# Optimization experiments

Hardware: AMD Instinct MI355X
Metric: run time of the kernel (lower is better)

The kernel has to match this reference:

```python
import jax, jax.numpy as jnp
import numpy as np

B, L, H, D, N, R, K = 1, 2048, 2048, 4096, 16, 128, 4


def setup_inputs() -> dict:
    key = jax.random.key(0)
    ks = jax.random.split(key, 10)
    s = 0.02
    x = jax.random.normal(ks[0], (B, L, H), dtype=jnp.float32)
    W_in = jax.random.normal(ks[1], (H, 2 * D), dtype=jnp.float32) * s
    conv_w = jax.random.normal(ks[2], (K, D), dtype=jnp.float32) * s  # depthwise causal conv
    conv_b = jnp.zeros((D,), dtype=jnp.float32)
    W_x = jax.random.normal(ks[3], (D, R + 2 * N), dtype=jnp.float32) * s
    W_dt = jax.random.normal(ks[4], (R, D), dtype=jnp.float32) * (R ** -0.5)
    # dt bias initialized so softplus(b_dt) ~ dt in [1e-3, 1e-1]
    dt = jnp.exp(jax.random.uniform(ks[5], (D,)) * (np.log(0.1) - np.log(1e-3)) + np.log(1e-3))
    b_dt = dt + jnp.log(-jnp.expm1(-dt))
    A_log = jnp.broadcast_to(jnp.log(jnp.arange(1, N + 1, dtype=jnp.float32)), (D, N))
    D_param = jnp.ones((D,), dtype=jnp.float32)
    W_out = jax.random.normal(ks[6], (D, H), dtype=jnp.float32) * s
    return {"x": x, "W_in": W_in, "conv_w": conv_w, "conv_b": conv_b,
            "W_x": W_x, "W_dt": W_dt, "b_dt": b_dt, "A_log": A_log,
            "D_param": D_param, "W_out": W_out}


def _mamba_fwd(x, W_in, conv_w, conv_b, W_x, W_dt, b_dt, A_log, D_param, W_out):
    silu = jax.nn.silu
    # in_proj then chunk into hidden / gate: [B,L,D] each
    proj = x @ W_in
    hs, gate = jnp.split(proj, 2, axis=-1)
    # causal depthwise conv along sequence (pad K-1 on the left)
    hs_pad = jnp.pad(hs, ((0, 0), (K - 1, 0), (0, 0)))
    conv = sum(hs_pad[:, k:k + L, :] * conv_w[k] for k in range(K)) + conv_b
    hs = silu(conv)  # [B,L,D]
    # ssm parameters
    ssm_p = hs @ W_x  # [B,L,R+2N]
    dt_in, Bm, Cm = jnp.split(ssm_p, [R, R + N], axis=-1)
    dt = jax.nn.softplus(dt_in @ W_dt + b_dt)  # [B,L,D]
    A = -jnp.exp(A_log)  # [D,N]
    dA = jnp.exp(dt[..., None] * A)                       # [B,L,D,N]
    dBu = dt[..., None] * Bm[:, :, None, :] * hs[..., None]  # [B,L,D,N]

    def step(s, inp):
        dA_t, dBu_t, C_t = inp
        s = dA_t * s + dBu_t                 # [B,D,N]
        y = jnp.einsum('bdn,bn->bd', s, C_t)
        return s, y

    s0 = jnp.zeros((B, D, N), dtype=x.dtype)
    xs = (jnp.moveaxis(dA, 1, 0), jnp.moveaxis(dBu, 1, 0), jnp.moveaxis(Cm, 1, 0))
    _, ys = jax.lax.scan(step, s0, xs)       # [L,B,D]
    y = jnp.moveaxis(ys, 0, 1)               # [B,L,D]
    y = y + hs * D_param
    y = y * silu(gate)
    return y @ W_out                          # [B,L,H]


def reference(x, W_in, conv_w, conv_b, W_x, W_dt, b_dt, A_log, D_param, W_out):
    return _mamba_fwd(x, W_in, conv_w, conv_b, W_x, W_dt, b_dt, A_log, D_param, W_out)
```

## Files before the change

### kernel.cpp

```cpp
#include <hip/hip_runtime.h>
#include <hip/hip_bf16.h>

typedef short short8 __attribute__((ext_vector_type(8)));
typedef float floatx4 __attribute__((ext_vector_type(4)));
using bf16 = __hip_bfloat16;

static constexpr int L = 2048, H = 2048, D = 4096, NS = 16, R = 128, KC = 4;
static constexpr int CCH = 64, TCH = L / CCH;
static constexpr int KSP = 16, KCHUNK = 4096 / KSP;
static constexpr int ZOUT = 4, KOUT = 4096 / ZOUT;

__device__ __forceinline__ void g2lds16(const void* g, void* l) {
  __builtin_amdgcn_global_load_lds((const __attribute__((address_space(1))) unsigned int*)g,
                                   (__attribute__((address_space(3))) unsigned int*)l,
                                   16, 0, 0);
}

__global__ void cast_f2b(const float* __restrict__ in, bf16* __restrict__ out, int n) {
  int i = blockIdx.x * 256 + threadIdx.x;
  if (i < n) out[i] = __float2bfloat16(in[i]);
}

__global__ void transpose_cast(const float* __restrict__ in, bf16* __restrict__ out,
                               int Rr, int Cc) {
  __shared__ float tile[32][33];
  int c0 = blockIdx.x * 32, r0 = blockIdx.y * 32;
  int tx = threadIdx.x, ty = threadIdx.y;
#pragma unroll
  for (int i = 0; i < 32; i += 8)
    tile[ty + i][tx] = in[(size_t)(r0 + ty + i) * Cc + (c0 + tx)];
  __syncthreads();
#pragma unroll
  for (int i = 0; i < 32; i += 8)
    out[(size_t)(c0 + ty + i) * Rr + (r0 + tx)] = __float2bfloat16(tile[tx][ty + i]);
}

template <int MODE>
__global__ __launch_bounds__(512, 2) void gemm256(
    const bf16* __restrict__ A, int lda,
    const bf16* __restrict__ Bt, int ldb,
    bf16* __restrict__ Cb, bf16* __restrict__ Cb2, int ldc, int K) {
  __shared__ short As[4 * 8192];
  __shared__ short Bs[4 * 8192];

  const int gx = gridDim.x, gy = gridDim.y;
  const int orig = blockIdx.y * gx + blockIdx.x;
  const int xcd = orig & 7;
  const int rr = orig >> 3;
  const int rn = gx >> 2, rm = gy >> 1;
  const int tn = (xcd & 3) * rn + (rr % rn);
  const int tm = (xcd >> 2) * rm + (rr / rn);
  const int n0 = tn * 256, m0 = tm * 256;
  const int kbeg = (MODE == 3) ? blockIdx.z * K : 0;
  const int NT = K >> 6;

  const int tid = threadIdx.x;
  const int lane = tid & 63;
  const int w = tid >> 6;
  const int wm2 = w >> 2, wn4 = w & 3;
  const int lr = lane & 15, kq = lane >> 4;
  const int swzr = ((lane >> 3) & 1) << 1;
  const int ardo = (wm2 * 128 + lr) * 32 + (kq ^ swzr) * 8;
  const int brdo = (wn4 * 64 + lr) * 32 + (kq ^ swzr) * 8;
  const int srow = w * 16 + (lane >> 2);
  const int swzs = ((lane >> 5) & 1) << 1;
  const int scol = ((lane & 3) ^ swzs) * 8;

  floatx4 acc[8][4];
#pragma unroll
  for (int i = 0; i < 8; i++)
#pragma unroll
    for (int j = 0; j < 4; j++)
#pragma unroll
      for (int r = 0; r < 4; r++) acc[i][j][r] = 0.f;

  auto stageA = [&](short* pan, int kc) {
    const bf16* g = A + (size_t)(m0 + srow) * lda + (kbeg + kc + scol);
    g2lds16(g, pan + w * 512);
    g2lds16(g + (size_t)128 * lda, pan + 4096 + w * 512);
  };
  auto stageB = [&](short* pan, int kc) {
    const bf16* g = Bt + (size_t)(n0 + srow) * ldb + (kbeg + kc + scol);
    g2lds16(g, pan + w * 512);
    g2lds16(g + (size_t)128 * ldb, pan + 4096 + w * 512);
  };

#define LDA4(pan, base)                                               \
  _Pragma("unroll") for (int ii = 0; ii < 4; ii++)                    \
      af[ii] = *(const short8*)((pan) + ardo + ((base) + ii) * 512);
#define LDB4(pan)                                                     \
  _Pragma("unroll") for (int jj = 0; jj < 4; jj++)                    \
      bfr[jj] = *(const short8*)((pan) + brdo + jj * 512);
#define MFMA4(base)                                                   \
  _Pragma("unroll") for (int ii = 0; ii < 4; ii++)                    \
      _Pragma("unroll") for (int jj = 0; jj < 4; jj++)                \
          acc[(base) + ii][jj] = __builtin_amdgcn_mfma_f32_16x16x32_bf16( \
              af[ii], bfr[jj], acc[(base) + ii][jj], 0, 0, 0);
#define LGK0() asm volatile("s_waitcnt lgkmcnt(0)" ::: "memory");
#define VMW(n) asm volatile("s_waitcnt vmcnt(" #n ")" ::: "memory");
#define BAR() __builtin_amdgcn_s_barrier();

  stageA(As + 0 * 8192, 0);
  stageB(Bs + 0 * 8192, 0);
  stageA(As + 1 * 8192, 32);
  stageB(Bs + 1 * 8192, 32);
  stageA(As + 2 * 8192, 64);
  stageB(Bs + 2 * 8192, 64);
  VMW(8);
  BAR();

#define GTILE(t, par)                                                      \
  {                                                                        \
    short* Ak0 = As + (par) * 16384;                                       \
    short* Bk0 = Bs + (par) * 16384;                                       \
    short* Ak1 = Ak0 + 8192;                                               \
    short* Bk1 = Bk0 + 8192;                                               \
    short* An1 = As + (1 - (par)) * 16384 + 8192;                          \
    short* Bn1 = Bs + (1 - (par)) * 16384 + 8192;                          \
    short8 af[4], bfr[4];                                                  \
                                                \
    LDB4(Bk0); LDA4(Ak0, 0);                                               \
    if ((t) + 1 < NT) stageA(An1, ((t) + 1) * 64 + 32);                    \
    __builtin_amdgcn_s_setprio(1); MFMA4(0); __builtin_amdgcn_s_setprio(0);\
    BAR();                                                                 \
                                   \
    LDA4(Ak0, 4);                                                          \
    if ((t) + 1 < NT) stageB(Bn1, ((t) + 1) * 64 + 32);                    \
    __builtin_amdgcn_s_setprio(1); MFMA4(4); __builtin_amdgcn_s_setprio(0);\
    LGK0();                                                                \
    if ((t) < NT - 1) { VMW(8); } else { VMW(0); }      \
    BAR();                                                                 \
                                                \
    LDB4(Bk1); LDA4(Ak1, 0);                                               \
    if ((t) + 2 < NT) stageA(Ak0, ((t) + 2) * 64);                         \
    __builtin_amdgcn_s_setprio(1); MFMA4(0); __builtin_amdgcn_s_setprio(0);\
    BAR();                                                                 \
                                   \
    LDA4(Ak1, 4);                                                          \
    if ((t) + 2 < NT) stageB(Bk0, ((t) + 2) * 64);                         \
    __builtin_amdgcn_s_setprio(1); MFMA4(4); __builtin_amdgcn_s_setprio(0);\
    LGK0();                                                                \
                                                      \
    if ((t) < NT - 2) { VMW(8); }                                          \
    else if ((t) == NT - 2) { VMW(4); }                                    \
    else { VMW(0); }                                                       \
    BAR();                                                                 \
  }

  for (int t = 0; t < NT; t += 2) {
    GTILE(t, 0);
    GTILE(t + 1, 1);
  }
#undef GTILE
#undef BAR
#undef VMW
#undef LGK0
#undef MFMA4
#undef LDB4
#undef LDA4

  bf16* base = Cb;
  int coff = 0, ld = ldc;
  if (MODE == 2) {
    if (n0 >= D) { base = Cb2; coff = D; }
    ld = D;
  }
  if (MODE == 3) base = Cb + (size_t)blockIdx.z * L * ldc;
  const int rb = kq * 4;
#pragma unroll
  for (int i = 0; i < 8; i++)
#pragma unroll
    for (int j = 0; j < 4; j++) {
      int col = n0 + wn4 * 64 + j * 16 + lr - coff;
      int row = m0 + wm2 * 128 + i * 16 + rb;
#pragma unroll
      for (int r = 0; r < 4; r++)
        base[(size_t)(row + r) * ld + col] = __float2bfloat16(acc[i][j][r]);
    }
}

template <int MODE>
__global__ __launch_bounds__(256) void gemm_async(
    const bf16* __restrict__ A, int lda,
    const bf16* __restrict__ Bt, int ldb,
    bf16* __restrict__ Cb, bf16* __restrict__ Cb2, int ldc, int K) {
  __shared__ short As[2 * 128 * 32];
  __shared__ short Bs[2 * 128 * 32];
  const int m0 = blockIdx.y * 128, n0 = blockIdx.x * 128;
  const int kbeg = (MODE == 3) ? blockIdx.z * K : 0;
  const int tid = threadIdx.x;
  const int lane = tid & 63;
  const int wave = tid >> 6;
  const int wm = (wave >> 1) * 64, wn = (wave & 1) * 64;
  const int lr = lane & 15, kq = lane >> 4;
  const int sr = lane >> 2, sc = (lane & 3) * 8;

  const bf16* Ab = A + (size_t)(m0 + wave * 16 + sr) * lda + sc;
  const bf16* Bb = Bt + (size_t)(n0 + wave * 16 + sr) * ldb + sc;
  short* Asw = &As[wave * 16 * 32];
  short* Bsw = &Bs[wave * 16 * 32];

  floatx4 acc[4][4];
#pragma unroll
  for (int i = 0; i < 4; i++)
#pragma unroll
    for (int j = 0; j < 4; j++)
#pragma unroll
      for (int r = 0; r < 4; r++) acc[i][j][r] = 0.f;

  for (int k0 = kbeg; k0 < kbeg + K; k0 += 64) {
    __syncthreads();
#pragma unroll
    for (int h = 0; h < 2; h++) {
      int kk = k0 + h * 32;
#pragma unroll
      for (int j = 0; j < 2; j++) {
        g2lds16(Ab + (size_t)j * 64 * lda + kk, Asw + h * 4096 + j * 64 * 32);
        g2lds16(Bb + (size_t)j * 64 * ldb + kk, Bsw + h * 4096 + j * 64 * 32);
      }
    }
    __syncthreads();
#pragma unroll
    for (int h = 0; h < 2; h++) {
      short8 af[4], bfr[4];
#pragma unroll
      for (int i = 0; i < 4; i++)
        af[i] = *(const short8*)(&As[h * 4096 + (wm + i * 16 + lr) * 32 + kq * 8]);
#pragma unroll
      for (int j = 0; j < 4; j++)
        bfr[j] = *(const short8*)(&Bs[h * 4096 + (wn + j * 16 + lr) * 32 + kq * 8]);
#pragma unroll
      for (int i = 0; i < 4; i++)
#pragma unroll
        for (int j = 0; j < 4; j++)
          acc[i][j] = __builtin_amdgcn_mfma_f32_16x16x32_bf16(af[i], bfr[j], acc[i][j], 0, 0, 0);
    }
  }

  bf16* base = Cb;
  int coff = 0, ld = ldc;
  if (MODE == 2) {
    if (n0 >= D) { base = Cb2; coff = D; }
    ld = D;
  }
  if (MODE == 3) base = Cb + (size_t)blockIdx.z * L * ldc;
  const int rb = kq * 4;
#pragma unroll
  for (int i = 0; i < 4; i++)
#pragma unroll
    for (int j = 0; j < 4; j++) {
      int col = n0 + wn + j * 16 + lr - coff;
      int row = m0 + wm + i * 16 + rb;
#pragma unroll
      for (int r = 0; r < 4; r++)
        base[(size_t)(row + r) * ld + col] = __float2bfloat16(acc[i][j][r]);
    }
}

__global__ void out_reduce(const unsigned short* __restrict__ P, float* __restrict__ out) {
  int i = blockIdx.x * 256 + threadIdx.x;
  const size_t LH = (size_t)L * H;
  float acc[8];
#pragma unroll
  for (int e = 0; e < 8; e++) acc[e] = 0.f;
#pragma unroll
  for (int z = 0; z < ZOUT; z++) {
    short8 v = *(const short8*)(P + z * LH + (size_t)i * 8);
#pragma unroll
    for (int e = 0; e < 8; e++)
      acc[e] += __uint_as_float(((unsigned)(unsigned short)v[e]) << 16);
  }
#pragma unroll
  for (int q = 0; q < 2; q++) {
    floatx4 o;
#pragma unroll
    for (int r = 0; r < 4; r++) o[r] = acc[q * 4 + r];
    *(floatx4*)(out + (size_t)i * 8 + q * 4) = o;
  }
}

__global__ __launch_bounds__(256) void gemm_splitk(
    const bf16* __restrict__ A, int lda,
    const bf16* __restrict__ Bt, int ldb,
    float* __restrict__ P, int ldc, int N) {
  __shared__ short As[128 * 40];
  __shared__ short Bs[128 * 40];
  const int m0 = blockIdx.y * 128, n0 = blockIdx.x * 128;
  const int kbeg = blockIdx.z * KCHUNK;
  float* C = P + (size_t)blockIdx.z * L * ldc;
  const int tid = threadIdx.x;
  const int lane = tid & 63;
  const int wave = tid >> 6;
  const int wm = (wave >> 1) * 64, wn = (wave & 1) * 64;
  const int lr = lane & 15, kq = lane >> 4;
  const int srow = tid >> 2, scol = (tid & 3) * 8;

  floatx4 acc[4][4];
#pragma unroll
  for (int i = 0; i < 4; i++)
#pragma unroll
    for (int j = 0; j < 4; j++)
#pragma unroll
      for (int r = 0; r < 4; r++) acc[i][j][r] = 0.f;

  for (int k0 = kbeg; k0 < kbeg + KCHUNK; k0 += 32) {
    __syncthreads();
#pragma unroll
    for (int h = 0; h < 2; h++) {
      int r = srow + h * 64;
      short8 va = *(const short8*)((const short*)A + (size_t)(m0 + r) * lda + k0 + scol);
      *(short8*)(&As[r * 40 + scol]) = va;
    }
#pragma unroll
    for (int h = 0; h < 2; h++) {
      int r = srow + h * 64;
      short8 vb;
      if ((n0 + r) < N) {
        vb = *(const short8*)((const short*)Bt + (size_t)(n0 + r) * ldb + k0 + scol);
      } else {
#pragma unroll
        for (int q = 0; q < 8; q++) vb[q] = 0;
      }
      *(short8*)(&Bs[r * 40 + scol]) = vb;
    }
    __syncthreads();
    short8 af[4], bfr[4];
#pragma unroll
    for (int i = 0; i < 4; i++)
      af[i] = *(const short8*)(&As[(wm + i * 16 + lr) * 40 + kq * 8]);
#pragma unroll
    for (int j = 0; j < 4; j++)
      bfr[j] = *(const short8*)(&Bs[(wn + j * 16 + lr) * 40 + kq * 8]);
#pragma unroll
    for (int i = 0; i < 4; i++)
#pragma unroll
      for (int j = 0; j < 4; j++)
        acc[i][j] = __builtin_amdgcn_mfma_f32_16x16x32_bf16(af[i], bfr[j], acc[i][j], 0, 0, 0);
  }

  const int rb = kq * 4;
#pragma unroll
  for (int i = 0; i < 4; i++)
#pragma unroll
    for (int j = 0; j < 4; j++) {
      int col = n0 + wn + j * 16 + lr;
      if (col >= N) continue;
      int row = m0 + wm + i * 16 + rb;
#pragma unroll
      for (int r = 0; r < 4; r++)
        C[(size_t)(row + r) * ldc + col] = acc[i][j][r];
    }
}

__global__ void splitk_reduce(const float* __restrict__ P, float* __restrict__ ssmp,
                              bf16* __restrict__ dtin) {
  int idx = blockIdx.x * 256 + threadIdx.x;
  float s = 0.f;
#pragma unroll
  for (int z = 0; z < KSP; z++) s += P[(size_t)z * L * 160 + idx];
  ssmp[idx] = s;
  int t = idx / 160, c = idx - t * 160;
  if (c < R) dtin[t * R + c] = __float2bfloat16(s);
}

__global__ void conv_silu(const bf16* __restrict__ projh,
                          const float* __restrict__ conv_w, const float* __restrict__ conv_b,
                          bf16* __restrict__ hs_b) {
  int idx = blockIdx.x * 256 + threadIdx.x;
  int d = idx & (D - 1), t = idx >> 12;
  float acc = conv_b[d];
#pragma unroll
  for (int k = 0; k < KC; k++) {
    int tt = t + k - (KC - 1);
    if (tt >= 0) acc += __bfloat162float(projh[(size_t)tt * D + d]) * conv_w[k * D + d];
  }
  float s = acc / (1.f + __expf(-acc));
  hs_b[idx] = __float2bfloat16(s);
}

__device__ __forceinline__ float softplusf(float v) {
  return (v > 20.f) ? v : log1pf(__expf(v));
}

__global__ __launch_bounds__(256) void scan_phase1(
    const bf16* __restrict__ dtraw, const float* __restrict__ b_dt,
    const bf16* __restrict__ hs_b, const float* __restrict__ ssmp,
    const float* __restrict__ A_log,
    float* __restrict__ sdt_out, float* __restrict__ S_out) {
  const int d = blockIdx.x * 256 + threadIdx.x;
  const int c = blockIdx.y;
  float An[NS];
#pragma unroll
  for (int n = 0; n < NS; n++) An[n] = -__expf(A_log[d * NS + n]);
  const float bdt = b_dt[d];
  float s[NS];
#pragma unroll
  for (int n = 0; n < NS; n++) s[n] = 0.f;
  float sdt = 0.f;
  const int t0 = c * TCH;
#pragma unroll 2
  for (int t = t0; t < t0 + TCH; t++) {
    float dtv = softplusf(__bfloat162float(dtraw[(size_t)t * D + d]) + bdt);
    float hsv = __bfloat162float(hs_b[(size_t)t * D + d]);
    sdt += dtv;
    float u = dtv * hsv;
    const float* Bp = ssmp + (size_t)t * 160 + 128;
#pragma unroll
    for (int n = 0; n < NS; n++) {
      float dA = __expf(An[n] * dtv);
      s[n] = dA * s[n] + Bp[n] * u;
    }
  }
  sdt_out[(size_t)c * D + d] = sdt;
  float* Sp = S_out + ((size_t)c * D + d) * NS;
#pragma unroll
  for (int n = 0; n < NS; n += 4)
    *(floatx4*)(Sp + n) = *(floatx4*)(s + n);
}

__global__ __launch_bounds__(256) void scan_phase2(
    const float* __restrict__ sdt, const float* __restrict__ S,
    const float* __restrict__ A_log, float* __restrict__ I) {
  int g = blockIdx.x * 256 + threadIdx.x;
  int d = g >> 4;
  float An = -__expf(A_log[g]);
  float cur = 0.f;
  float sdt_n = sdt[d];
  float S_n = S[g];
  for (int c = 0; c < CCH; c++) {
    float sdt_c = sdt_n, S_c = S_n;
    if (c + 1 < CCH) {
      sdt_n = sdt[(size_t)(c + 1) * D + d];
      S_n = S[(size_t)(c + 1) * D * NS + g];
    }
    I[(size_t)c * D * NS + g] = cur;
    cur = __expf(An * sdt_c) * cur + S_c;
  }
}

__global__ __launch_bounds__(256) void scan_phase3(
    const bf16* __restrict__ dtraw, const float* __restrict__ b_dt,
    const bf16* __restrict__ hs_b, const float* __restrict__ ssmp,
    const bf16* __restrict__ gate_b, const float* __restrict__ A_log,
    const float* __restrict__ D_param, const float* __restrict__ I,
    bf16* __restrict__ y_b) {
  const int d = blockIdx.x * 256 + threadIdx.x;
  const int c = blockIdx.y;
  float An[NS];
#pragma unroll
  for (int n = 0; n < NS; n++) An[n] = -__expf(A_log[d * NS + n]);
  const float bdt = b_dt[d];
  const float Dp = D_param[d];
  float s[NS];
  const float* Ip = I + ((size_t)c * D + d) * NS;
#pragma unroll
  for (int n = 0; n < NS; n += 4)
    *(floatx4*)(s + n) = *(const floatx4*)(Ip + n);
  const int t0 = c * TCH;
#pragma unroll 2
  for (int t = t0; t < t0 + TCH; t++) {
    float dtv = softplusf(__bfloat162float(dtraw[(size_t)t * D + d]) + bdt);
    float hsv = __bfloat162float(hs_b[(size_t)t * D + d]);
    float u = dtv * hsv;
    const float* Bp = ssmp + (size_t)t * 160 + 128;
    const float* Cp = ssmp + (size_t)t * 160 + 144;
    float y = 0.f;
#pragma unroll
    for (int n = 0; n < NS; n++) {
      float dA = __expf(An[n] * dtv);
      s[n] = dA * s[n] + Bp[n] * u;
      y += s[n] * Cp[n];
    }
    float gv = __bfloat162float(gate_b[(size_t)t * D + d]);
    float yv = (y + hsv * Dp) * (gv / (1.f + __expf(-gv)));
    y_b[(size_t)t * D + d] = __float2bfloat16(yv);
  }
}

extern "C" void kernel_launch(void* const* d_in, const int* in_sizes, int n_in,
                              void* d_out, int out_size, void* d_ws, size_t ws_size,
                              hipStream_t stream) {
  const float* x      = (const float*)d_in[0];
  const float* W_in   = (const float*)d_in[1];
  const float* conv_w = (const float*)d_in[2];
  const float* conv_b = (const float*)d_in[3];
  const float* W_x    = (const float*)d_in[4];
  const float* W_dt   = (const float*)d_in[5];
  const float* b_dt   = (const float*)d_in[6];
  const float* A_log  = (const float*)d_in[7];
  const float* D_par  = (const float*)d_in[8];
  const float* W_out  = (const float*)d_in[9];
  float* outp = (float*)d_out;

  char* ws = (char*)d_ws;
  size_t off = 0;
  auto alloc = [&](size_t bytes) {
    char* p = ws + off;
    off += (bytes + 255) & ~(size_t)255;
    return (void*)p;
  };
  bf16*  gate_b  = (bf16*) alloc((size_t)L * D * 2);
  bf16*  hs_b    = (bf16*) alloc((size_t)L * D * 2);
  float* ssmp    = (float*)alloc((size_t)L * 160 * 4);
  bf16*  dtin_b  = (bf16*) alloc((size_t)L * R * 2);
  bf16*  dtbuf_b = (bf16*) alloc((size_t)L * D * 2);
  bf16*  y_b     = (bf16*) alloc((size_t)L * D * 2);
  bf16*  WoutT   = (bf16*) alloc((size_t)H * D * 2);
  float* sdt     = (float*)alloc((size_t)CCH * D * 4);
  float* Sbuf    = (float*)alloc((size_t)CCH * D * NS * 4);
  float* Ibuf    = (float*)alloc((size_t)CCH * D * NS * 4);
  size_t tbase = off;
  bf16*  x_b     = (bf16*) alloc((size_t)L * H * 2);
  bf16*  WinT    = (bf16*) alloc((size_t)2 * D * H * 2);
  bf16*  WxT     = (bf16*) alloc((size_t)160 * D * 2);
  bf16*  WdtT    = (bf16*) alloc((size_t)D * R * 2);
  bf16*  projh_b = (bf16*) alloc((size_t)L * D * 2);
  float* part    = (float*)alloc((size_t)KSP * L * 160 * 4);
  bf16*  part2   = (bf16*)(ws + tbase);

  cast_f2b<<<(L * H) / 256, 256, 0, stream>>>(x, x_b, L * H);

  dim3 tb(32, 8);
  transpose_cast<<<dim3((2 * D) / 32, H / 32), tb, 0, stream>>>(W_in, WinT, H, 2 * D);
  transpose_cast<<<dim3(H / 32, D / 32), tb, 0, stream>>>(W_out, WoutT, D, H);
  transpose_cast<<<dim3(160 / 32, D / 32), tb, 0, stream>>>(W_x, WxT, D, 160);
  transpose_cast<<<dim3(D / 32, R / 32), tb, 0, stream>>>(W_dt, WdtT, R, D);

  gemm256<2><<<dim3((2 * D) / 256, L / 256), 512, 0, stream>>>(
      x_b, H, WinT, H, projh_b, gate_b, D, H);
  conv_silu<<<(L * D) / 256, 256, 0, stream>>>(projh_b, conv_w, conv_b, hs_b);
  gemm_splitk<<<dim3(2, L / 128, KSP), 256, 0, stream>>>(
      hs_b, D, WxT, D, part, 160, 160);
  splitk_reduce<<<(L * 160) / 256, 256, 0, stream>>>(part, ssmp, dtin_b);
  gemm_async<1><<<dim3(D / 128, L / 128), 256, 0, stream>>>(
      dtin_b, R, WdtT, R, dtbuf_b, nullptr, D, R);

  scan_phase1<<<dim3(D / 256, CCH), 256, 0, stream>>>(
      dtbuf_b, b_dt, hs_b, ssmp, A_log, sdt, Sbuf);
  scan_phase2<<<(D * NS) / 256, 256, 0, stream>>>(sdt, Sbuf, A_log, Ibuf);
  scan_phase3<<<dim3(D / 256, CCH), 256, 0, stream>>>(
      dtbuf_b, b_dt, hs_b, ssmp, gate_b, A_log, D_par, Ibuf, y_b);

  gemm256<3><<<dim3(H / 256, L / 256, ZOUT), 512, 0, stream>>>(
      y_b, D, WoutT, D, part2, nullptr, H, KOUT);
  out_reduce<<<(L * H) / (256 * 8), 256, 0, stream>>>((const unsigned short*)part2, outp);
}
```

Measured before the change: 472.5 us.

## Restructure GEMM main loop into four-stage ring with one barrier pair per k-slice

Replaces the two-half-tile GTILE schedule (split A loads and four barriers per 32-wide k-slice) with a four-slot LDS ring. Each phase waits on vmcnt, loads all 8 A fragments and 4 B fragments, issues the next global-to-LDS stage into a free slot, then runs all 32 MFMAs at once. This aims to cut barrier count and interleaving overhead in the large bf16 GEMMs. The cost is more live A registers and less fine-grained overlap of LDS reads with MFMAs, and the vmcnt accounting at the loop tail has to stay correct.

```diff
diff --git a/kernel.cpp b/kernel.cpp
--- a/kernel.cpp
+++ b/kernel.cpp
@@ -85,79 +85,55 @@
     g2lds16(g + (size_t)128 * ldb, pan + 4096 + w * 512);
   };
 
-#define LDA4(pan, base)                                               \
-  _Pragma("unroll") for (int ii = 0; ii < 4; ii++)                    \
-      af[ii] = *(const short8*)((pan) + ardo + ((base) + ii) * 512);
+#define LDA8(pan)                                                     \
+  _Pragma("unroll") for (int ii = 0; ii < 8; ii++)                    \
+      af[ii] = *(const short8*)((pan) + ardo + ii * 512);
 #define LDB4(pan)                                                     \
   _Pragma("unroll") for (int jj = 0; jj < 4; jj++)                    \
       bfr[jj] = *(const short8*)((pan) + brdo + jj * 512);
-#define MFMA4(base)                                                   \
-  _Pragma("unroll") for (int ii = 0; ii < 4; ii++)                    \
+#define MFMA32()                                                      \
+  _Pragma("unroll") for (int ii = 0; ii < 8; ii++)                    \
       _Pragma("unroll") for (int jj = 0; jj < 4; jj++)                \
-          acc[(base) + ii][jj] = __builtin_amdgcn_mfma_f32_16x16x32_bf16( \
-              af[ii], bfr[jj], acc[(base) + ii][jj], 0, 0, 0);
+          acc[ii][jj] = __builtin_amdgcn_mfma_f32_16x16x32_bf16(      \
+              af[ii], bfr[jj], acc[ii][jj], 0, 0, 0);
 #define LGK0() asm volatile("s_waitcnt lgkmcnt(0)" ::: "memory");
 #define VMW(n) asm volatile("s_waitcnt vmcnt(" #n ")" ::: "memory");
 #define BAR() __builtin_amdgcn_s_barrier();
 
-  stageA(As + 0 * 8192, 0);
-  stageB(Bs + 0 * 8192, 0);
-  stageA(As + 1 * 8192, 32);
-  stageB(Bs + 1 * 8192, 32);
-  stageA(As + 2 * 8192, 64);
-  stageB(Bs + 2 * 8192, 64);
-  VMW(8);
-  BAR();
-
-#define GTILE(t, par)                                                      \
+  stageA(As + 0 * 8192, 0);   stageB(Bs + 0 * 8192, 0);
+  stageA(As + 1 * 8192, 32);  stageB(Bs + 1 * 8192, 32);
+  stageA(As + 2 * 8192, 64);  stageB(Bs + 2 * 8192, 64);
+
+#define GPH(sR, sS, kcS, vmn, scond)                                       \
   {                                                                        \
-    short* Ak0 = As + (par) * 16384;                                       \
-    short* Bk0 = Bs + (par) * 16384;                                       \
-    short* Ak1 = Ak0 + 8192;                                               \
-    short* Bk1 = Bk0 + 8192;                                               \
-    short* An1 = As + (1 - (par)) * 16384 + 8192;                          \
-    short* Bn1 = Bs + (1 - (par)) * 16384 + 8192;                          \
-    short8 af[4], bfr[4];                                                  \
-                                                \
-    LDB4(Bk0); LDA4(Ak0, 0);                                               \
-    if ((t) + 1 < NT) stageA(An1, ((t) + 1) * 64 + 32);                    \
-    __builtin_amdgcn_s_setprio(1); MFMA4(0); __builtin_amdgcn_s_setprio(0);\
+    VMW(vmn);                                                              \
     BAR();                                                                 \
-                                   \
-    LDA4(Ak0, 4);                                                          \
-    if ((t) + 1 < NT) stageB(Bn1, ((t) + 1) * 64 + 32);                    \
-    __builtin_amdgcn_s_setprio(1); MFMA4(4); __builtin_amdgcn_s_setprio(0);\
+    short8 af[8], bfr[4];                                                  \
+    LDA8(As + (sR) * 8192);                                                \
+    LDB4(Bs + (sR) * 8192);                                                \
+    if (scond) { stageA(As + (sS) * 8192, kcS); stageB(Bs + (sS) * 8192, kcS); } \
+    BAR();                                                                 \
     LGK0();                                                                \
-    if ((t) < NT - 1) { VMW(8); } else { VMW(0); }      \
-    BAR();                                                                 \
-                                                \
-    LDB4(Bk1); LDA4(Ak1, 0);                                               \
-    if ((t) + 2 < NT) stageA(Ak0, ((t) + 2) * 64);                         \
-    __builtin_amdgcn_s_setprio(1); MFMA4(0); __builtin_amdgcn_s_setprio(0);\
-    BAR();                                                                 \
-                                   \
-    LDA4(Ak1, 4);                                                          \
-    if ((t) + 2 < NT) stageB(Bk0, ((t) + 2) * 64);                         \
-    __builtin_amdgcn_s_setprio(1); MFMA4(4); __builtin_amdgcn_s_setprio(0);\
-    LGK0();                                                                \
-                                                      \
-    if ((t) < NT - 2) { VMW(8); }                                          \
-    else if ((t) == NT - 2) { VMW(4); }                                    \
-    else { VMW(0); }                                                       \
-    BAR();                                                                 \
+    __builtin_amdgcn_s_setprio(1); MFMA32(); __builtin_amdgcn_s_setprio(0);\
   }
 
   for (int t = 0; t < NT; t += 2) {
-    GTILE(t, 0);
-    GTILE(t + 1, 1);
-  }
-#undef GTILE
+    if (t < NT - 1) { GPH(0, 3, (t + 1) * 64 + 32, 8, 1); }
+    else            { GPH(0, 3, 0, 4, 0); }
+    if (t < NT - 1) { GPH(1, 0, (t + 2) * 64, 8, (t + 2 < NT)); }
+    else            { GPH(1, 0, 0, 0, 0); }
+    if (t + 1 < NT - 1) { GPH(2, 1, (t + 2) * 64 + 32, 8, 1); }
+    else                { GPH(2, 1, 0, 4, 0); }
+    if (t + 1 < NT - 1) { GPH(3, 2, (t + 3) * 64, 8, (t + 3 < NT)); }
+    else                { GPH(3, 2, 0, 0, 0); }
+  }
+#undef GPH
 #undef BAR
 #undef VMW
 #undef LGK0
-#undef MFMA4
+#undef MFMA32
 #undef LDB4
-#undef LDA4
+#undef LDA8
 
   bf16* base = Cb;
   int coff = 0, ld = ldc;
@@ -513,7 +489,7 @@
   bf16*  x_b     = (bf16*) alloc((size_t)L * H * 2);
   bf16*  WinT    = (bf16*) alloc((size_t)2 * D * H * 2);
   bf16*  WxT     = (bf16*) alloc((size_t)160 * D * 2);
-  bf16*  WdtT    = (bf16*) alloc((size_t)D * R * 2);
+  bf16*  WdtT   = (bf16*) alloc((size_t)D * R * 2);
   bf16*  projh_b = (bf16*) alloc((size_t)L * D * 2);
   float* part    = (float*)alloc((size_t)KSP * L * 160 * 4);
   bf16*  part2   = (bf16*)(ws + tbase);
```

Result: slower. 852.2 us (+80.4%).
